# Kernel tuning notes

Measured on AMD Instinct MI355X. Metric: run time of the kernel, lower is better.

Reference implementation:

```python
import jax, jax.numpy as jnp
import numpy as np

N_HEAD = 16
NEG = -1.0e9


def setup_inputs() -> dict:
    key = jax.random.key(0)
    k1, k2, k3 = jax.random.split(key, 3)
    B, T, C = 4, 2048, 1024
    x = jax.random.normal(k1, (B, T, C), dtype=jnp.float32)
    # torch Linear(C, 3C, bias=False): weight [3C, C], y = x @ W.T
    w_attn = jax.random.normal(k2, (3 * C, C), dtype=jnp.float32) * (1.0 / np.sqrt(C))
    w_proj = jax.random.normal(k3, (C, C), dtype=jnp.float32) * (1.0 / np.sqrt(C))
    return {"x": x, "w_attn": w_attn, "w_proj": w_proj}


def reference(x, w_attn, w_proj):
    B, T, C = x.shape
    hd = C // N_HEAD
    qkv = x @ w_attn.T  # [B,T,3C]
    q, k, v = jnp.split(qkv, 3, axis=2)
    # [B,T,C] -> [B,H,T,hd]
    q = q.reshape(B, T, N_HEAD, hd).transpose(0, 2, 1, 3)
    k = k.reshape(B, T, N_HEAD, hd).transpose(0, 2, 1, 3)
    v = v.reshape(B, T, N_HEAD, hd).transpose(0, 2, 1, 3)
    att = jnp.einsum('bhqd,bhkd->bhqk', q, k) * (1.0 / np.sqrt(hd))
    causal = jnp.tril(jnp.ones((T, T), dtype=bool))
    att = jnp.where(causal[None, None, :, :], att, NEG)
    att = jax.nn.softmax(att, axis=-1)
    y = jnp.einsum('bhqk,bhkd->bhqd', att, v)  # [B,H,T,hd]
    y = y.transpose(0, 2, 1, 3).reshape(B, T, C)
    return y @ w_proj.T
```

## Files before the change

kernel.cpp:

```cpp
#include <hip/hip_runtime.h>
#include <hip/hip_bf16.h>

typedef __bf16 bf16x8_t __attribute__((ext_vector_type(8)));
typedef __bf16 bf16x4_t __attribute__((ext_vector_type(4)));
typedef float f32x4_t __attribute__((ext_vector_type(4)));
typedef float f32x16_t __attribute__((ext_vector_type(16)));

__device__ __forceinline__ void gload_lds16(const void* g, void* l) {
    __builtin_amdgcn_global_load_lds((const __attribute__((address_space(1))) void*)g,
                                     (__attribute__((address_space(3))) void*)l, 16, 0, 0);
}

__device__ __forceinline__ unsigned pk_bf16(float a, float b) {
    unsigned r;
    asm("v_cvt_pk_bf16_f32 %0, %1, %2" : "=v"(r) : "v"(a), "v"(b));
    return r;
}

__global__ void f2bf3_kernel(const float* __restrict__ x, const float* __restrict__ wa,
                             const float* __restrict__ wp, __bf16* __restrict__ xb,
                             __bf16* __restrict__ wab, __bf16* __restrict__ wpb) {
    int i = blockIdx.x * blockDim.x + threadIdx.x;
    const float* in; __bf16* out; int off;
    if (i < 2097152)      { in = x;  out = xb;  off = i; }
    else if (i < 2883584) { in = wa; out = wab; off = i - 2097152; }
    else                  { in = wp; out = wpb; off = i - 2883584; }
    float4 v = *(const float4*)(in + off * 4);
    bf16x4_t o;
    o[0] = (__bf16)v.x; o[1] = (__bf16)v.y; o[2] = (__bf16)v.z; o[3] = (__bf16)v.w;
    *(bf16x4_t*)(out + off * 4) = o;
}

__global__ __launch_bounds__(512, 2) void gemm1_m201(const __bf16* __restrict__ A,
                                                     const __bf16* __restrict__ Bt,
                                                     __bf16* __restrict__ Cqk,
                                                     __bf16* __restrict__ Vg,
                                                     int M, int N, int K) {
    __shared__ __bf16 As[2][256 * 64];
    __shared__ __bf16 Bs[2][192 * 64];

    const int tid  = threadIdx.x;
    const int lane = tid & 63;
    const int wid  = tid >> 6;
    const int wm   = wid >> 2;
    const int wn   = wid & 3;

    int fl = blockIdx.x;
    fl = (fl & 7) * (gridDim.x >> 3) + (fl >> 3);
    const int m0 = (fl >> 4) * 256;
    const int n0 = (fl & 15) * 192;

    const int lr = lane & 15;
    const int lg = lane >> 4;
    const int cr = lg * 4;
    const int srow = lane >> 3;
    const int gcol = (((lane & 7) ^ srow) << 3);

    f32x4_t acc[8][3];
#pragma unroll
    for (int i = 0; i < 8; ++i)
#pragma unroll
        for (int j = 0; j < 3; ++j)
            acc[i][j] = (f32x4_t){0.f, 0.f, 0.f, 0.f};

    const int NT = K >> 6;
    const int NI = NT >> 1;

    bf16x8_t af[4][2], bf0[2][2], bf1[1][2];

    auto stA = [&](int kt, int buf, int half) {
        const __bf16* Ab = A + (size_t)m0 * K + (size_t)kt * 64;
        const int s0 = half * 16 + wid, s1 = s0 + 8;
        gload_lds16(Ab + (size_t)(s0 * 8 + srow) * K + gcol, &As[buf][s0 * 512]);
        gload_lds16(Ab + (size_t)(s1 * 8 + srow) * K + gcol, &As[buf][s1 * 512]);
    };
    auto stBlo = [&](int kt, int buf) {
        const __bf16* Bb = Bt + (size_t)n0 * K + (size_t)kt * 64;
        gload_lds16(Bb + (size_t)(wid * 8 + srow) * K + gcol, &Bs[buf][wid * 512]);
        gload_lds16(Bb + (size_t)((wid + 8) * 8 + srow) * K + gcol, &Bs[buf][(wid + 8) * 512]);
    };
    auto stBhi = [&](int kt, int buf) {
        const __bf16* Bb = Bt + (size_t)n0 * K + (size_t)kt * 64;
        gload_lds16(Bb + (size_t)((wid + 16) * 8 + srow) * K + gcol, &Bs[buf][(wid + 16) * 512]);
    };
    auto dsA = [&](const __bf16* Ab, int mfh) {
#pragma unroll
        for (int mf = 0; mf < 4; ++mf)
#pragma unroll
            for (int kk = 0; kk < 2; ++kk) {
                const int row = wm * 128 + (mfh * 4 + mf) * 16 + lr;
                const int g   = kk * 4 + lg;
                af[mf][kk] = *(const bf16x8_t*)&Ab[row * 64 + ((g ^ (row & 7)) << 3)];
            }
    };
    auto dsB0 = [&](const __bf16* Bb) {
#pragma unroll
        for (int nfp = 0; nfp < 2; ++nfp)
#pragma unroll
            for (int kk = 0; kk < 2; ++kk) {
                const int row = wn * 48 + nfp * 16 + lr;
                const int g   = kk * 4 + lg;
                bf0[nfp][kk] = *(const bf16x8_t*)&Bb[row * 64 + ((g ^ (row & 7)) << 3)];
            }
    };
    auto dsB1 = [&](const __bf16* Bb) {
#pragma unroll
        for (int kk = 0; kk < 2; ++kk) {
            const int row = wn * 48 + 2 * 16 + lr;
            const int g   = kk * 4 + lg;
            bf1[0][kk] = *(const bf16x8_t*)&Bb[row * 64 + ((g ^ (row & 7)) << 3)];
        }
    };
    auto MF0 = [&](int mfh) {
        __builtin_amdgcn_s_setprio(1);
#pragma unroll
        for (int mf = 0; mf < 4; ++mf)
#pragma unroll
            for (int nfp = 0; nfp < 2; ++nfp) {
                const int ai = mfh * 4 + mf;
                acc[ai][nfp] = __builtin_amdgcn_mfma_f32_16x16x32_bf16(af[mf][0], bf0[nfp][0], acc[ai][nfp], 0, 0, 0);
                acc[ai][nfp] = __builtin_amdgcn_mfma_f32_16x16x32_bf16(af[mf][1], bf0[nfp][1], acc[ai][nfp], 0, 0, 0);
            }
        __builtin_amdgcn_s_setprio(0);
    };
    auto MF1 = [&](int mfh) {
        __builtin_amdgcn_s_setprio(1);
#pragma unroll
        for (int mf = 0; mf < 4; ++mf) {
            const int ai = mfh * 4 + mf;
            acc[ai][2] = __builtin_amdgcn_mfma_f32_16x16x32_bf16(af[mf][0], bf1[0][0], acc[ai][2], 0, 0, 0);
            acc[ai][2] = __builtin_amdgcn_mfma_f32_16x16x32_bf16(af[mf][1], bf1[0][1], acc[ai][2], 0, 0, 0);
        }
        __builtin_amdgcn_s_setprio(0);
    };

#define BAR() __builtin_amdgcn_s_barrier()
#define LGK0() asm volatile("s_waitcnt lgkmcnt(0)" ::: "memory")

    stA(0, 0, 0); stA(0, 0, 1); stBlo(0, 0); stBhi(0, 0);
    stBlo(1, 1); stBhi(1, 1);
    asm volatile("s_waitcnt vmcnt(3)" ::: "memory");
    BAR();

    for (int it = 0; it < NI; ++it) {
        const int t1 = 2 * it + 1, t2 = 2 * it + 2, t3 = 2 * it + 3;
        const bool lastit = (it == NI - 1);

        dsA(As[0], 0); dsB0(Bs[0]);
        stA(t1, 1, 0);
        BAR(); LGK0();
        MF0(0);
        BAR();

        dsB1(Bs[0]);
        stA(t1, 1, 1);
        BAR(); LGK0();
        MF1(0);
        BAR();

        dsA(As[0], 1);
        if (!lastit) stBlo(t2, 0);
        BAR(); LGK0();
        MF0(1);
        BAR();

        if (!lastit) stBhi(t2, 0);
        if (lastit) asm volatile("s_waitcnt vmcnt(0)" ::: "memory");
        else        asm volatile("s_waitcnt vmcnt(3)" ::: "memory");
        BAR();
        MF1(1);
        BAR();

        dsA(As[1], 0); dsB0(Bs[1]);
        if (!lastit) stA(t2, 0, 0);
        BAR(); LGK0();
        MF0(0);
        BAR();

        dsB1(Bs[1]);
        if (!lastit) stA(t2, 0, 1);
        BAR(); LGK0();
        MF1(0);
        BAR();

        dsA(As[1], 1);
        if (!lastit) stBlo(t3, 1);
        BAR(); LGK0();
        MF0(1);
        BAR();

        if (!lastit) stBhi(t3, 1);
        if (lastit) asm volatile("s_waitcnt vmcnt(0)" ::: "memory");
        else        asm volatile("s_waitcnt vmcnt(3)" ::: "memory");
        BAR();
        MF1(1);
        BAR();
    }
#undef BAR
#undef LGK0

#pragma unroll
    for (int mf = 0; mf < 8; ++mf) {
        const int row0 = m0 + wm * 128 + mf * 16 + cr;
        const int bb   = row0 >> 11;
        const int tt   = row0 & 2047;
#pragma unroll
        for (int nf = 0; nf < 3; ++nf) {
            const int colb = n0 + wn * 48 + nf * 16;
            if (colb < 2048) {
#pragma unroll
                for (int r = 0; r < 4; ++r)
                    Cqk[(size_t)(row0 + r) * 2048 + colb + lr] = (__bf16)acc[mf][nf][r];
            } else {
                const int c3 = colb + lr - 2048;
                const int hh = c3 >> 6, dd = c3 & 63;
                bf16x4_t pv;
#pragma unroll
                for (int r = 0; r < 4; ++r) pv[r] = (__bf16)acc[mf][nf][r];
                *(bf16x4_t*)&Vg[((size_t)(bb * 16 + hh) * 64 + dd) * 2048 + tt] = pv;
            }
        }
    }
}

template <typename OutT>
__global__ __launch_bounds__(256) void gemm_bt(const __bf16* __restrict__ A,
                                               const __bf16* __restrict__ Bt,
                                               OutT* __restrict__ C,
                                               int M, int N, int K) {
    __shared__ __bf16 As[128 * 32];
    __shared__ __bf16 Bs[128 * 32];

    const int tid  = threadIdx.x;
    const int lane = tid & 63;
    const int wid  = tid >> 6;
    const int wm   = wid >> 1;
    const int wn   = wid & 1;

    const int nwg = gridDim.x * gridDim.y;
    int fl = blockIdx.y * gridDim.x + blockIdx.x;
    fl = (fl & 7) * (nwg >> 3) + (fl >> 3);
    const int m0 = (fl / gridDim.x) * 128;
    const int n0 = (fl % gridDim.x) * 128;

    const int lr = lane & 15;
    const int lk = (lane >> 4) * 8;
    const int cr = (lane >> 4) * 4;

    f32x4_t acc[4][4];
    for (int i = 0; i < 4; ++i)
        for (int j = 0; j < 4; ++j)
            acc[i][j] = (f32x4_t){0.f, 0.f, 0.f, 0.f};

    for (int k0 = 0; k0 < K; k0 += 32) {
        __syncthreads();
        for (int i = 0; i < 2; ++i) {
            int flat = i * 256 + tid;
            int row  = flat >> 2;
            int col  = (flat & 3) * 8;
            gload_lds16(&A[(size_t)(m0 + row) * K + k0 + col], &As[(size_t)(i * 256 + wid * 64) * 8]);
            gload_lds16(&Bt[(size_t)(n0 + row) * K + k0 + col], &Bs[(size_t)(i * 256 + wid * 64) * 8]);
        }
        __syncthreads();

        bf16x8_t af[4], bfr[4];
        for (int mf = 0; mf < 4; ++mf)
            af[mf] = *(const bf16x8_t*)&As[(wm * 64 + mf * 16 + lr) * 32 + lk];
        for (int nf = 0; nf < 4; ++nf)
            bfr[nf] = *(const bf16x8_t*)&Bs[(wn * 64 + nf * 16 + lr) * 32 + lk];
        for (int mf = 0; mf < 4; ++mf)
            for (int nf = 0; nf < 4; ++nf)
                acc[mf][nf] = __builtin_amdgcn_mfma_f32_16x16x32_bf16(af[mf], bfr[nf], acc[mf][nf], 0, 0, 0);
    }

    for (int mf = 0; mf < 4; ++mf)
        for (int nf = 0; nf < 4; ++nf)
            for (int r = 0; r < 4; ++r) {
                int row = m0 + wm * 64 + mf * 16 + cr + r;
                int col = n0 + wn * 64 + nf * 16 + lr;
                C[(size_t)row * N + col] = (OutT)acc[mf][nf][r];
            }
}

__global__ __launch_bounds__(256, 2) void attn_kernel(const __bf16* __restrict__ qkv,
                                                      const __bf16* __restrict__ Vg,
                                                      __bf16* __restrict__ y) {
    const int T = 2048, LD = 2048;
    const int orig = blockIdx.x;
    const int bidx = ((orig & 7) << 6) + (orig >> 3);
    const int pair = bidx & 7;
    const int h    = (bidx >> 3) & 15;
    const int b    = bidx >> 7;

    __shared__ __bf16 Ks[2][128 * 64];
    __shared__ __bf16 Vt[2][64 * 128];

    const int tid  = threadIdx.x;
    const int lane = tid & 63;
    const int w    = tid >> 6;
    const int l31  = lane & 31;
    const int hi   = lane >> 5;

    const __bf16* qg  = qkv + (size_t)b * T * LD + h * 64;
    const __bf16* kg  = qg + 1024;
    const __bf16* Vgb = Vg + (size_t)(b * 16 + h) * 64 * 2048;

    const float CE    = 0.125f * 1.44269504f;
    const float DEFER = 8.0f;

    const int kc = tid & 7;
    const int kr8 = tid >> 3;
    const int kslot = (kc ^ (kr8 & 7)) << 3;
    const int vc = tid & 15;
    const int vd8 = tid >> 4;
    const int vslot = (vc ^ (vd8 & 7)) << 3;

    bf16x8_t ones8;
#pragma unroll
    for (int j = 0; j < 8; ++j) ones8[j] = (__bf16)1.0f;

    for (int pass = 0; pass < 2; ++pass) {
        const int qs  = pass ? 15 - pair : pair;
        const int qt0 = qs * 128;
        const int nt  = qs + 1;
        const int qgl = qt0 + w * 32 + l31;

        bf16x8_t qreg[4];
#pragma unroll
        for (int ks = 0; ks < 4; ++ks) {
            bf16x8_t qr = *(const bf16x8_t*)&qg[(size_t)qgl * LD + ks * 16 + 8 * hi];
            union { unsigned u[4]; bf16x8_t v; } pq;
#pragma unroll
            for (int j = 0; j < 4; ++j)
                pq.u[j] = pk_bf16((float)qr[2 * j] * CE, (float)qr[2 * j + 1] * CE);
            qreg[ks] = pq.v;
        }

        bf16x8_t kreg[4], vreg[4];
#pragma unroll
        for (int jj = 0; jj < 4; ++jj)
            kreg[jj] = *(const bf16x8_t*)&kg[(size_t)(kr8 + 32 * jj) * LD + kc * 8];
#pragma unroll
        for (int jj = 0; jj < 4; ++jj)
            vreg[jj] = *(const bf16x8_t*)&Vgb[(size_t)(vd8 + 16 * jj) * 2048 + vc * 8];

        f32x16_t o0 = (f32x16_t)(0.f), o1 = (f32x16_t)(0.f);
        f32x16_t o2 = (f32x16_t)(0.f);
        float m_r = -3.0e38f;

        __syncthreads();

        for (int t = 0; t < nt; ++t) {
            __bf16* Kb = Ks[t & 1];
            __bf16* Vb = Vt[t & 1];

#pragma unroll
            for (int jj = 0; jj < 4; ++jj)
                *(bf16x8_t*)&Kb[(kr8 + 32 * jj) * 64 + kslot] = kreg[jj];
#pragma unroll
            for (int jj = 0; jj < 4; ++jj)
                *(bf16x8_t*)&Vb[(vd8 + 16 * jj) * 128 + vslot] = vreg[jj];

            __syncthreads();

            if (t + 1 < nt) {
                const size_t kb0 = (size_t)(t + 1) * 128;
#pragma unroll
                for (int jj = 0; jj < 4; ++jj)
                    kreg[jj] = *(const bf16x8_t*)&kg[(kb0 + kr8 + 32 * jj) * LD + kc * 8];
#pragma unroll
                for (int jj = 0; jj < 4; ++jj)
                    vreg[jj] = *(const bf16x8_t*)&Vgb[(size_t)(vd8 + 16 * jj) * 2048 + kb0 + vc * 8];
            }

            f32x16_t s[4];
            __builtin_amdgcn_s_setprio(1);
#pragma unroll
            for (int kb = 0; kb < 4; ++kb) {
                const int key = kb * 32 + l31;
                const int sw7 = key & 7;
                s[kb] = (f32x16_t)(0.f);
#pragma unroll
                for (int ks = 0; ks < 4; ++ks) {
                    bf16x8_t kf = *(const bf16x8_t*)&Kb[key * 64 + (((2 * ks + hi) ^ sw7) << 3)];
                    s[kb] = __builtin_amdgcn_mfma_f32_32x32x16_bf16(kf, qreg[ks], s[kb], 0, 0, 0);
                }
            }
            __builtin_amdgcn_s_setprio(0);

            if (t == nt - 1) {
                const int ql = w * 32 + l31;
#pragma unroll
                for (int kb = 0; kb < 4; ++kb)
#pragma unroll
                    for (int r = 0; r < 16; ++r) {
                        const int key = kb * 32 + (r & 3) + 8 * (r >> 2) + 4 * hi;
                        if (key > ql) s[kb][r] = -1.0e30f;
                    }
            }

            float pm = -3.0e38f;
#pragma unroll
            for (int kb = 0; kb < 4; ++kb) {
                float a = fmaxf(fmaxf(s[kb][0], s[kb][1]), s[kb][2]);
                a = fmaxf(fmaxf(a, s[kb][3]), s[kb][4]);
                a = fmaxf(fmaxf(a, s[kb][5]), s[kb][6]);
                a = fmaxf(fmaxf(a, s[kb][7]), s[kb][8]);
                a = fmaxf(fmaxf(a, s[kb][9]), s[kb][10]);
                a = fmaxf(fmaxf(a, s[kb][11]), s[kb][12]);
                a = fmaxf(fmaxf(a, s[kb][13]), s[kb][14]);
                a = fmaxf(a, s[kb][15]);
                pm = fmaxf(pm, a);
            }

            if (!__all(pm <= m_r + DEFER)) {
                pm = fmaxf(pm, __shfl_xor(pm, 32));
                const float mn    = fmaxf(m_r, pm);
                const float alpha = exp2f(m_r - mn);
                o2[0] *= alpha;
#pragma unroll
                for (int r = 0; r < 16; ++r) { o0[r] *= alpha; o1[r] *= alpha; }
                m_r = mn;
            }
            const float mr = m_r;

#pragma unroll
            for (int kb = 0; kb < 4; ++kb)
#pragma unroll
                for (int r = 0; r < 16; ++r)
                    s[kb][r] = exp2f(s[kb][r] - mr);

            __builtin_amdgcn_s_setprio(1);
#pragma unroll
            for (int ks = 0; ks < 8; ++ks) {
                const int kb = ks >> 1;
                const int rb = 8 * (ks & 1);
                unsigned L0 = pk_bf16(s[kb][rb + 0], s[kb][rb + 1]);
                unsigned L1 = pk_bf16(s[kb][rb + 2], s[kb][rb + 3]);
                unsigned H0 = pk_bf16(s[kb][rb + 4], s[kb][rb + 5]);
                unsigned H1 = pk_bf16(s[kb][rb + 6], s[kb][rb + 7]);
                asm("v_permlane32_swap_b32 %0, %1" : "+v"(L0), "+v"(H0));
                asm("v_permlane32_swap_b32 %0, %1" : "+v"(L1), "+v"(H1));
                union { unsigned u[4]; bf16x8_t v; } uf;
                uf.u[0] = L0; uf.u[1] = L1; uf.u[2] = H0; uf.u[3] = H1;
                const int gv = 2 * ks + hi;
                {
                    const int d = l31;
                    bf16x8_t vf = *(const bf16x8_t*)&Vb[d * 128 + ((gv ^ (d & 7)) << 3)];
                    o0 = __builtin_amdgcn_mfma_f32_32x32x16_bf16(vf, uf.v, o0, 0, 0, 0);
                }
                {
                    const int d = 32 + l31;
                    bf16x8_t vf = *(const bf16x8_t*)&Vb[d * 128 + ((gv ^ (d & 7)) << 3)];
                    o1 = __builtin_amdgcn_mfma_f32_32x32x16_bf16(vf, uf.v, o1, 0, 0, 0);
                }
                o2 = __builtin_amdgcn_mfma_f32_32x32x16_bf16(ones8, uf.v, o2, 0, 0, 0);
            }
            __builtin_amdgcn_s_setprio(0);
        }

        const float inv = 1.0f / o2[0];
        __bf16* yrow = y + (size_t)(b * T + qgl) * 1024 + h * 64;
#pragma unroll
        for (int tq = 0; tq < 4; ++tq) {
            bf16x4_t ov0, ov1;
#pragma unroll
            for (int u = 0; u < 4; ++u) {
                ov0[u] = (__bf16)(o0[tq * 4 + u] * inv);
                ov1[u] = (__bf16)(o1[tq * 4 + u] * inv);
            }
            const int dl = 8 * tq + 4 * hi;
            *(bf16x4_t*)&yrow[dl]      = ov0;
            *(bf16x4_t*)&yrow[32 + dl] = ov1;
        }
    }
}

extern "C" void kernel_launch(void* const* d_in, const int* in_sizes, int n_in,
                              void* d_out, int out_size, void* d_ws, size_t ws_size,
                              hipStream_t stream) {
    const float* x      = (const float*)d_in[0];
    const float* w_attn = (const float*)d_in[1];
    const float* w_proj = (const float*)d_in[2];
    float* out = (float*)d_out;

    char* ws = (char*)d_ws;
    __bf16* xb   = (__bf16*)(ws);
    __bf16* wab  = (__bf16*)(ws + 16777216);
    __bf16* wpb  = (__bf16*)(ws + 23068672);
    __bf16* qkvb = (__bf16*)(ws + 25165824);
    __bf16* yb   = (__bf16*)(ws + 58720256);
    __bf16* Vg   = (__bf16*)(ws + 75497472);

    f2bf3_kernel<<<12288, 256, 0, stream>>>(x, w_attn, w_proj, xb, wab, wpb);

    gemm1_m201<<<512, 512, 0, stream>>>(xb, wab, qkvb, Vg, 8192, 3072, 1024);

    attn_kernel<<<512, 256, 0, stream>>>(qkvb, Vg, yb);

    gemm_bt<float><<<dim3(8, 64), 256, 0, stream>>>(yb, wpb, out, 8192, 1024, 1024);
}
```

Baseline: 173.9 us.

## Replace output projection GEMM with double-buffered 256x128 pipelined kernel

Replaces the simple 128x128 single-buffered output projection GEMM with a 512-thread 256x128 tile kernel. It uses K=64 double-buffered LDS stages with XOR-swizzled layout, interleaves global-to-LDS loads between MFMA phases, and raises wave priority around the MFMA bursts. The aim is to overlap memory loads with compute, avoid LDS bank conflicts and raise data reuse. In exchange it uses more LDS and registers, hard-codes N=1024 for the output stride, and relies on a hand-tuned barrier and waitcnt schedule.

```diff
diff --git a/kernel.cpp b/kernel.cpp
--- a/kernel.cpp
+++ b/kernel.cpp
@@ -223,63 +223,179 @@
     }
 }
 
-template <typename OutT>
-__global__ __launch_bounds__(256) void gemm_bt(const __bf16* __restrict__ A,
-                                               const __bf16* __restrict__ Bt,
-                                               OutT* __restrict__ C,
-                                               int M, int N, int K) {
-    __shared__ __bf16 As[128 * 32];
-    __shared__ __bf16 Bs[128 * 32];
+__global__ __launch_bounds__(512, 2) void gemm2_m201(const __bf16* __restrict__ A,
+                                                     const __bf16* __restrict__ Bt,
+                                                     float* __restrict__ C,
+                                                     int M, int N, int K) {
+    __shared__ __bf16 As[2][256 * 64];
+    __shared__ __bf16 Bs[2][128 * 64];
 
     const int tid  = threadIdx.x;
     const int lane = tid & 63;
     const int wid  = tid >> 6;
-    const int wm   = wid >> 1;
-    const int wn   = wid & 1;
-
-    const int nwg = gridDim.x * gridDim.y;
-    int fl = blockIdx.y * gridDim.x + blockIdx.x;
-    fl = (fl & 7) * (nwg >> 3) + (fl >> 3);
-    const int m0 = (fl / gridDim.x) * 128;
-    const int n0 = (fl % gridDim.x) * 128;
+    const int wm   = wid >> 2;
+    const int wn   = wid & 3;
+
+    int fl = blockIdx.x;
+    fl = (fl & 7) * (gridDim.x >> 3) + (fl >> 3);
+    const int m0 = (fl >> 3) * 256;
+    const int n0 = (fl & 7) * 128;
 
     const int lr = lane & 15;
-    const int lk = (lane >> 4) * 8;
-    const int cr = (lane >> 4) * 4;
-
-    f32x4_t acc[4][4];
-    for (int i = 0; i < 4; ++i)
-        for (int j = 0; j < 4; ++j)
+    const int lg = lane >> 4;
+    const int cr = lg * 4;
+    const int srow = lane >> 3;
+    const int gcol = (((lane & 7) ^ srow) << 3);
+
+    f32x4_t acc[8][2];
+#pragma unroll
+    for (int i = 0; i < 8; ++i)
+#pragma unroll
+        for (int j = 0; j < 2; ++j)
             acc[i][j] = (f32x4_t){0.f, 0.f, 0.f, 0.f};
 
-    for (int k0 = 0; k0 < K; k0 += 32) {
-        __syncthreads();
-        for (int i = 0; i < 2; ++i) {
-            int flat = i * 256 + tid;
-            int row  = flat >> 2;
-            int col  = (flat & 3) * 8;
-            gload_lds16(&A[(size_t)(m0 + row) * K + k0 + col], &As[(size_t)(i * 256 + wid * 64) * 8]);
-            gload_lds16(&Bt[(size_t)(n0 + row) * K + k0 + col], &Bs[(size_t)(i * 256 + wid * 64) * 8]);
-        }
-        __syncthreads();
-
-        bf16x8_t af[4], bfr[4];
+    const int NT = K >> 6;
+    const int NI = NT >> 1;
+
+    bf16x8_t af[4][2], bf0[1][2], bf1[1][2];
+
+    auto stA = [&](int kt, int buf, int half) {
+        const __bf16* Ab = A + (size_t)m0 * K + (size_t)kt * 64;
+        const int s0 = half * 16 + wid, s1 = s0 + 8;
+        gload_lds16(Ab + (size_t)(s0 * 8 + srow) * K + gcol, &As[buf][s0 * 512]);
+        gload_lds16(Ab + (size_t)(s1 * 8 + srow) * K + gcol, &As[buf][s1 * 512]);
+    };
+    auto stBlo = [&](int kt, int buf) {
+        const __bf16* Bb = Bt + (size_t)n0 * K + (size_t)kt * 64;
+        gload_lds16(Bb + (size_t)(wid * 8 + srow) * K + gcol, &Bs[buf][wid * 512]);
+    };
+    auto stBhi = [&](int kt, int buf) {
+        const __bf16* Bb = Bt + (size_t)n0 * K + (size_t)kt * 64;
+        gload_lds16(Bb + (size_t)((wid + 8) * 8 + srow) * K + gcol, &Bs[buf][(wid + 8) * 512]);
+    };
+    auto dsA = [&](const __bf16* Ab, int mfh) {
+#pragma unroll
         for (int mf = 0; mf < 4; ++mf)
-            af[mf] = *(const bf16x8_t*)&As[(wm * 64 + mf * 16 + lr) * 32 + lk];
-        for (int nf = 0; nf < 4; ++nf)
-            bfr[nf] = *(const bf16x8_t*)&Bs[(wn * 64 + nf * 16 + lr) * 32 + lk];
-        for (int mf = 0; mf < 4; ++mf)
-            for (int nf = 0; nf < 4; ++nf)
-                acc[mf][nf] = __builtin_amdgcn_mfma_f32_16x16x32_bf16(af[mf], bfr[nf], acc[mf][nf], 0, 0, 0);
+#pragma unroll
+            for (int kk = 0; kk < 2; ++kk) {
+                const int row = wm * 128 + (mfh * 4 + mf) * 16 + lr;
+                const int g   = kk * 4 + lg;
+                af[mf][kk] = *(const bf16x8_t*)&Ab[row * 64 + ((g ^ (row & 7)) << 3)];
+            }
+    };
+    auto dsB0 = [&](const __bf16* Bb) {
+#pragma unroll
+        for (int kk = 0; kk < 2; ++kk) {
+            const int row = wn * 32 + lr;
+            const int g   = kk * 4 + lg;
+            bf0[0][kk] = *(const bf16x8_t*)&Bb[row * 64 + ((g ^ (row & 7)) << 3)];
+        }
+    };
+    auto dsB1 = [&](const __bf16* Bb) {
+#pragma unroll
+        for (int kk = 0; kk < 2; ++kk) {
+            const int row = wn * 32 + 16 + lr;
+            const int g   = kk * 4 + lg;
+            bf1[0][kk] = *(const bf16x8_t*)&Bb[row * 64 + ((g ^ (row & 7)) << 3)];
+        }
+    };
+    auto MF0 = [&](int mfh) {
+        __builtin_amdgcn_s_setprio(1);
+#pragma unroll
+        for (int mf = 0; mf < 4; ++mf) {
+            const int ai = mfh * 4 + mf;
+            acc[ai][0] = __builtin_amdgcn_mfma_f32_16x16x32_bf16(af[mf][0], bf0[0][0], acc[ai][0], 0, 0, 0);
+            acc[ai][0] = __builtin_amdgcn_mfma_f32_16x16x32_bf16(af[mf][1], bf0[0][1], acc[ai][0], 0, 0, 0);
+        }
+        __builtin_amdgcn_s_setprio(0);
+    };
+    auto MF1 = [&](int mfh) {
+        __builtin_amdgcn_s_setprio(1);
+#pragma unroll
+        for (int mf = 0; mf < 4; ++mf) {
+            const int ai = mfh * 4 + mf;
+            acc[ai][1] = __builtin_amdgcn_mfma_f32_16x16x32_bf16(af[mf][0], bf1[0][0], acc[ai][1], 0, 0, 0);
+            acc[ai][1] = __builtin_amdgcn_mfma_f32_16x16x32_bf16(af[mf][1], bf1[0][1], acc[ai][1], 0, 0, 0);
+        }
+        __builtin_amdgcn_s_setprio(0);
+    };
+
+#define BAR() __builtin_amdgcn_s_barrier()
+#define LGK0() asm volatile("s_waitcnt lgkmcnt(0)" ::: "memory")
+
+    stA(0, 0, 0); stA(0, 0, 1); stBlo(0, 0); stBhi(0, 0);
+    stBlo(1, 1); stBhi(1, 1);
+    asm volatile("s_waitcnt vmcnt(2)" ::: "memory");
+    BAR();
+
+    for (int it = 0; it < NI; ++it) {
+        const int t1 = 2 * it + 1, t2 = 2 * it + 2, t3 = 2 * it + 3;
+        const bool lastit = (it == NI - 1);
+
+        dsA(As[0], 0); dsB0(Bs[0]);
+        stA(t1, 1, 0);
+        BAR(); LGK0();
+        MF0(0);
+        BAR();
+
+        dsB1(Bs[0]);
+        stA(t1, 1, 1);
+        BAR(); LGK0();
+        MF1(0);
+        BAR();
+
+        dsA(As[0], 1);
+        if (!lastit) stBlo(t2, 0);
+        BAR(); LGK0();
+        MF0(1);
+        BAR();
+
+        if (!lastit) stBhi(t2, 0);
+        if (lastit) asm volatile("s_waitcnt vmcnt(0)" ::: "memory");
+        else        asm volatile("s_waitcnt vmcnt(2)" ::: "memory");
+        BAR();
+        MF1(1);
+        BAR();
+
+        dsA(As[1], 0); dsB0(Bs[1]);
+        if (!lastit) stA(t2, 0, 0);
+        BAR(); LGK0();
+        MF0(0);
+        BAR();
+
+        dsB1(Bs[1]);
+        if (!lastit) stA(t2, 0, 1);
+        BAR(); LGK0();
+        MF1(0);
+        BAR();
+
+        dsA(As[1], 1);
+        if (!lastit) stBlo(t3, 1);
+        BAR(); LGK0();
+        MF0(1);
+        BAR();
+
+        if (!lastit) stBhi(t3, 1);
+        if (lastit) asm volatile("s_waitcnt vmcnt(0)" ::: "memory");
+        else        asm volatile("s_waitcnt vmcnt(2)" ::: "memory");
+        BAR();
+        MF1(1);
+        BAR();
     }
-
-    for (int mf = 0; mf < 4; ++mf)
-        for (int nf = 0; nf < 4; ++nf)
-            for (int r = 0; r < 4; ++r) {
-                int row = m0 + wm * 64 + mf * 16 + cr + r;
-                int col = n0 + wn * 64 + nf * 16 + lr;
-                C[(size_t)row * N + col] = (OutT)acc[mf][nf][r];
-            }
+#undef BAR
+#undef LGK0
+
+#pragma unroll
+    for (int mf = 0; mf < 8; ++mf) {
+        const int row0 = m0 + wm * 128 + mf * 16 + cr;
+#pragma unroll
+        for (int nf = 0; nf < 2; ++nf) {
+            const int col = n0 + wn * 32 + nf * 16 + lr;
+#pragma unroll
+            for (int r = 0; r < 4; ++r)
+                C[(size_t)(row0 + r) * 1024 + col] = acc[mf][nf][r];
+        }
+    }
 }
 
 __global__ __launch_bounds__(256, 2) void attn_kernel(const __bf16* __restrict__ qkv,
@@ -498,5 +614,5 @@
 
     attn_kernel<<<512, 256, 0, stream>>>(qkvb, Vg, yb);
 
-    gemm_bt<float><<<dim3(8, 64), 256, 0, stream>>>(yb, wpb, out, 8192, 1024, 1024);
+    gemm2_m201<<<256, 512, 0, stream>>>(yb, wpb, out, 8192, 1024, 1024);
 }
```

Measured after the change: 168.2 us (median of 2 runs). 1.03x faster.
